# Kernel optimization log

Measured on AMD Instinct MI355X. Metric: run time of the kernel, lower is better.

## Reference

```python
import jax, jax.numpy as jnp
import numpy as np
from math import pi as PI

K = 32
CUTOFF = 10.0
F = 128          # num_filters (also num_gaussians)
H = 256          # in_channels
N_CLASSES = 7
N_IND = 8
LOG2 = float(np.log(2.0))


def _ssp(x):
    # ShiftedSoftplus
    return jax.nn.softplus(x) - LOG2


def _gaussian_smearing(d):
    # d: [E, 1] -> [E, F]; torch_geometric GaussianSmearing(start=0, stop=cutoff)
    offset = jnp.linspace(0.0, CUTOFF, F, dtype=d.dtype)            # [F]
    coeff = -0.5 / (offset[1] - offset[0]) ** 2
    return jnp.exp(coeff * (d - offset[None, :]) ** 2)


def setup_inputs() -> dict:
    key = jax.random.key(0)
    ks = jax.random.split(key, 24)
    Nq, Nc, B = 8192, 16384, 8
    box = 20.0
    pos_query = jax.random.uniform(ks[0], (Nq, 3), dtype=jnp.float32) * box
    pos_ctx = jax.random.uniform(ks[1], (Nc, 3), dtype=jnp.float32) * box
    node_attr_ctx = jax.random.normal(ks[2], (Nc, H), dtype=jnp.float32)
    batch_query = jnp.sort(jax.random.randint(ks[3], (Nq,), 0, B)).astype(jnp.int32)
    batch_ctx = jnp.sort(jax.random.randint(ks[4], (Nc,), 0, B)).astype(jnp.int32)

    def lin_w(k, fin, fout):
        return (jax.random.normal(k, (fin, fout), dtype=jnp.float32) / np.sqrt(fin)).astype(jnp.float32)

    return {
        "pos_query": pos_query,
        "pos_ctx": pos_ctx,
        "node_attr_ctx": node_attr_ctx,
        "batch_query": batch_query,
        "batch_ctx": batch_ctx,
        "lin1_w": lin_w(ks[5], H, F),                 # bias=False
        "lin2_w": lin_w(ks[6], F, F),
        "lin2_b": jnp.zeros((F,), jnp.float32),
        "nn1_w": lin_w(ks[7], F, F),
        "nn1_b": jnp.zeros((F,), jnp.float32),
        "nn2_w": lin_w(ks[8], F, F),
        "nn2_b": jnp.zeros((F,), jnp.float32),
        "cls1_w": lin_w(ks[9], F, F),
        "cls1_b": jnp.zeros((F,), jnp.float32),
        "cls2_w": lin_w(ks[10], F, N_CLASSES),
        "cls2_b": jnp.zeros((N_CLASSES,), jnp.float32),
        "prop1_w": lin_w(ks[11], F, F),
        "prop1_b": jnp.zeros((F,), jnp.float32),
        "prop2_w": lin_w(ks[12], F, N_IND),
        "prop2_b": jnp.zeros((N_IND,), jnp.float32),
    }


def reference(pos_query, pos_ctx, node_attr_ctx, batch_query, batch_ctx,
              lin1_w, lin2_w, lin2_b, nn1_w, nn1_b, nn2_w, nn2_b,
              cls1_w, cls1_b, cls2_w, cls2_b, prop1_w, prop1_b, prop2_w, prop2_b):
    Nq = pos_query.shape[0]

    # --- batch-aware kNN: for each query, k nearest context points in same graph ---
    d2 = (jnp.sum(pos_query ** 2, -1)[:, None]
          + jnp.sum(pos_ctx ** 2, -1)[None, :]
          - 2.0 * (pos_query @ pos_ctx.T))                            # [Nq, Nc]
    same = batch_query[:, None] == batch_ctx[None, :]
    d2 = jnp.where(same, d2, jnp.inf)
    _, nbr = jax.lax.top_k(-d2, K)                                    # [Nq, K] ctx indices

    # --- gather neighbor data; each query owns exactly K contiguous edges ---
    diff = pos_query[:, None, :] - pos_ctx[nbr]                       # [Nq, K, 3]
    dist = jnp.sqrt(jnp.sum(diff ** 2, -1)).reshape(-1, 1)            # [E, 1]
    attr_j = node_attr_ctx[nbr].reshape(Nq * K, -1)                   # [E, H]

    # --- per-edge filter network on distance expansion ---
    W = _ssp(_gaussian_smearing(dist) @ nn1_w + nn1_b) @ nn2_w + nn2_b  # [E, F]

    h = (W * (attr_j @ lin1_w)) @ lin2_w + lin2_b                     # [E, F]

    # --- cosine cutoff envelope ---
    C = 0.5 * (jnp.cos(dist * (PI / CUTOFF)) + 1.0)
    C = C * (dist <= CUTOFF) * (dist >= 0.0)
    h = h * C                                                         # [E, F]

    # scatter_add by query index == sum over the K contiguous edges per query
    y = jnp.sum(h.reshape(Nq, K, F), axis=1)                          # [Nq, F]

    y_cls = _ssp(y @ cls1_w + cls1_b) @ cls2_w + cls2_b               # [Nq, 7]
    y_ind = _ssp(y @ prop1_w + prop1_b) @ prop2_w + prop2_b           # [Nq, 8]
    return (y_cls, y_ind)
```

## Files before the change

kernel.cpp:

```cpp
#include <hip/hip_runtime.h>
#include <hip/hip_fp16.h>
#include <math.h>

#define K 32
#define F 128
#define H 256
#define TAB 4096
#define QB 8
#define BMAX 16
#define RCUT2 100.0f
#define KBINS 64
#define BINCAP 2560
#define BCAP 128
#define FP 132
#define WRR 16

typedef _Float16 f16x8 __attribute__((ext_vector_type(8)));
typedef float f32x4 __attribute__((ext_vector_type(4)));

__device__ __forceinline__ float ssp(float x) {
    return fmaxf(x, 0.0f) + log1pf(expf(-fabsf(x))) - 0.69314718055994531f;
}

__device__ __forceinline__ float d2f4(float4 p, float qx, float qy, float qz) {
    float dx = qx - p.x;
    float dy = qy - p.y;
    float dz = qz - p.z;
    return fmaf(dz, dz, fmaf(dy, dy, dx * dx));
}

__global__ __launch_bounds__(256) void prep_kernel(const int* __restrict__ bc, int Nc,
                                                   int* __restrict__ ctx_start,
                                                   const float* __restrict__ posc,
                                                   float4* __restrict__ posc4,
                                                   const float* __restrict__ attr,
                                                   __half* __restrict__ attrh,
                                                   const float* __restrict__ lin1_w,
                                                   __half* __restrict__ bfragh,
                                                   int padB, int convB) {
    int blk = blockIdx.x;
    int tid = threadIdx.x;
    if (blk == 0) {
        if (tid <= BMAX) {
            int b = tid;
            int lo = 0, hi = Nc;
            while (lo < hi) {
                int mid = (lo + hi) >> 1;
                if (bc[mid] < b) lo = mid + 1; else hi = mid;
            }
            ctx_start[b] = lo;
        }
    } else if (blk <= padB) {
        int i = (blk - 1) * 256 + tid;
        if (i < Nc)
            posc4[i] = make_float4(posc[i * 3 + 0], posc[i * 3 + 1], posc[i * 3 + 2], 0.0f);
    } else if (blk <= padB + convB) {
        size_t base = ((size_t)(blk - 1 - padB) * 256 + tid) * 8;
        if (base < (size_t)Nc * H) {
            float4 v0 = *(const float4*)&attr[base];
            float4 v1 = *(const float4*)&attr[base + 4];
            __half2 h[4];
            h[0] = __floats2half2_rn(v0.x, v0.y);
            h[1] = __floats2half2_rn(v0.z, v0.w);
            h[2] = __floats2half2_rn(v1.x, v1.y);
            h[3] = __floats2half2_rn(v1.z, v1.w);
            *(float4*)&attrh[base] = *(float4*)h;
        }
    } else {
        int ts = blk - 1 - padB - convB;
        int t = ts >> 3, s = ts & 7;
        for (int e = tid; e < 512; e += 256) {
            int l = e >> 3, j = e & 7;
            int k = s * 32 + (l >> 4) * 8 + j;
            int col = (l & 15) + 16 * t;
            bfragh[(size_t)ts * 512 + e] = __float2half(lin1_w[k * F + col]);
        }
    }
}

__global__ __launch_bounds__(256) void feat_kernel(const __half* __restrict__ attrh_,
                                                   const __half* __restrict__ bfragh_,
                                                   __half* __restrict__ ctx_feat, int Nc) {
    const _Float16* attrh = (const _Float16*)attrh_;
    const _Float16* bfragh = (const _Float16*)bfragh_;
    int tid = threadIdx.x;
    int wave = tid >> 6;
    int lane = tid & 63;
    int r0 = blockIdx.x * 32;

    f32x4 acc[2][2] = {{{0.f,0.f,0.f,0.f},{0.f,0.f,0.f,0.f}},{{0.f,0.f,0.f,0.f},{0.f,0.f,0.f,0.f}}};

    int arow[2];
#pragma unroll
    for (int rt = 0; rt < 2; ++rt) {
        int row = r0 + rt * 16 + (lane & 15);
        arow[rt] = (row < Nc) ? row : (Nc - 1);
    }
    int kbase = (lane >> 4) * 8;

    for (int s = 0; s < 8; ++s) {
        f16x8 a0 = *(const f16x8*)(attrh + (size_t)arow[0] * H + s * 32 + kbase);
        f16x8 a1 = *(const f16x8*)(attrh + (size_t)arow[1] * H + s * 32 + kbase);
#pragma unroll
        for (int ct = 0; ct < 2; ++ct) {
            int t = 2 * wave + ct;
            f16x8 b = *(const f16x8*)(bfragh + ((size_t)(t * 8 + s) * 64 + lane) * 8);
            acc[0][ct] = __builtin_amdgcn_mfma_f32_16x16x32_f16(a0, b, acc[0][ct], 0, 0, 0);
            acc[1][ct] = __builtin_amdgcn_mfma_f32_16x16x32_f16(a1, b, acc[1][ct], 0, 0, 0);
        }
    }

#pragma unroll
    for (int rt = 0; rt < 2; ++rt) {
#pragma unroll
        for (int ct = 0; ct < 2; ++ct) {
            int col = (2 * wave + ct) * 16 + (lane & 15);
#pragma unroll
            for (int j = 0; j < 4; ++j) {
                int row = r0 + rt * 16 + (lane >> 4) * 4 + j;
                if (row < Nc)
                    ctx_feat[(size_t)row * F + col] = __float2half(acc[rt][ct][j]);
            }
        }
    }
}

__global__ __launch_bounds__(256) void knn_kernel(const float* __restrict__ posq,
                                                  const float4* __restrict__ posc4,
                                                  const int* __restrict__ bq,
                                                  const int* __restrict__ ctx_start,
                                                  int* __restrict__ nbr, int Nq) {
    __shared__ unsigned char sbin[4][BINCAP];
    __shared__ int hist[4][KBINS];
    __shared__ unsigned bkey[4][BCAP];
    __shared__ int bidx[4][BCAP];
    __shared__ int s_nwin[4], s_nbnd[4];

    int tid = threadIdx.x;
    int lane = tid & 63;
    int w = tid >> 6;
    int q = blockIdx.x * 4 + w;
    bool active = q < Nq;
    int qc = active ? q : 0;

    hist[w][lane] = 0;
    if (lane == 0) { s_nwin[w] = 0; s_nbnd[w] = 0; }

    float qx = posq[qc * 3 + 0];
    float qy = posq[qc * 3 + 1];
    float qz = posq[qc * 3 + 2];
    int b = bq[qc];
    int c0 = ctx_start[b];
    int c1 = ctx_start[b + 1];
    int seg = active ? (c1 - c0) : 0;
    __syncthreads();

    const float SCALE = (float)KBINS / RCUT2;
    int farc = -1;

    for (int i = lane; i < seg; i += 64) {
        float d2 = d2f4(posc4[c0 + i], qx, qy, qz);
        int bin = 255;
        if (d2 < RCUT2) {
            bin = (int)(d2 * SCALE);
            atomicAdd(&hist[w][bin], 1);
        }
        if (i < BINCAP) sbin[w][i] = (unsigned char)bin;
    }
    __syncthreads();

    int h = hist[w][lane];
    int inc = h;
#pragma unroll
    for (int off = 1; off < 64; off <<= 1) {
        int v = __shfl_up(inc, off);
        if (lane >= off) inc += v;
    }
    unsigned long long bal = __ballot(inc >= K);
    int T, below;
    if (bal) {
        T = __ffsll(bal) - 1;
        below = __shfl(inc, T) - __shfl(h, T);
    } else {
        T = KBINS;
        below = __shfl(inc, 63);
    }

    for (int i = lane; i < seg; i += 64) {
        int c = c0 + i;
        int bin;
        if (i < BINCAP) bin = sbin[w][i];
        else {
            float d2 = d2f4(posc4[c], qx, qy, qz);
            bin = (d2 < RCUT2) ? (int)(d2 * SCALE) : 255;
        }
        if (bin < T) {
            int p = atomicAdd(&s_nwin[w], 1);
            nbr[(size_t)q * K + p] = c;
        } else if (bin == T) {
            int p = atomicAdd(&s_nbnd[w], 1);
            if (p < BCAP) {
                float d2 = d2f4(posc4[c], qx, qy, qz);
                bkey[w][p] = __float_as_uint(d2);
                bidx[w][p] = c;
            }
        } else if (bin == 255) {
            farc = c;
        }
    }
#pragma unroll
    for (int off = 1; off < 64; off <<= 1) farc = max(farc, __shfl_xor(farc, off));
    if (farc < 0) farc = c0;
    __syncthreads();

    if (!active) return;
    int nb = min(s_nbnd[w], BCAP);
    int m = K - s_nwin[w];
    for (int it = 0; it < m; ++it) {
        unsigned long long bestkey = 0xFFFFFFFFFFFFFFFFull;
        int bestp = -1;
        for (int p = lane; p < nb; p += 64) {
            unsigned kk = bkey[w][p];
            if (kk != 0xFFFFFFFFu) {
                unsigned long long pk = ((unsigned long long)kk << 32) | (unsigned)bidx[w][p];
                if (pk < bestkey) { bestkey = pk; bestp = p; }
            }
        }
#pragma unroll
        for (int off = 1; off < 64; off <<= 1) {
            unsigned long long ok = __shfl_xor(bestkey, off);
            int op = __shfl_xor(bestp, off);
            if (ok < bestkey) { bestkey = ok; bestp = op; }
        }
        if (lane == 0) {
            if (bestp >= 0 && bestkey != 0xFFFFFFFFFFFFFFFFull) {
                nbr[(size_t)q * K + below + it] = (int)(bestkey & 0xFFFFFFFFu);
                bkey[w][bestp] = 0xFFFFFFFFu;
            } else {
                nbr[(size_t)q * K + below + it] = farc;
            }
        }
        __asm__ volatile("" ::: "memory");
    }
}

__global__ __launch_bounds__(256) void wtab_kernel(const float* __restrict__ nn1_w,
                                                   const float* __restrict__ nn1_b,
                                                   const float* __restrict__ nn2_w,
                                                   const float* __restrict__ nn2_b,
                                                   __half2* __restrict__ wt2h) {
    __shared__ float sg[17][F];
    __shared__ float st[17][F];
    int t0 = blockIdx.x * WRR;
    int tid = threadIdx.x;
    int f = tid & (F - 1);
    int g = tid >> 7;

    const float delta = 10.0f / 127.0f;
    const float coeff = -0.5f / (delta * delta);
    float off = (float)f * delta;
    for (int r = g; r < 17; r += 2) {
        float dist = (float)(t0 + r) * (10.0f / (float)TAB);
        float d = dist - off;
        sg[r][f] = expf(coeff * d * d);
    }
    __syncthreads();

    float acc[9];
#pragma unroll
    for (int r = 0; r < 9; ++r) acc[r] = 0.0f;
    for (int j = 0; j < F; j += 4) {
        float w0 = nn1_w[(j + 0) * F + f];
        float w1 = nn1_w[(j + 1) * F + f];
        float w2 = nn1_w[(j + 2) * F + f];
        float w3 = nn1_w[(j + 3) * F + f];
#pragma unroll
        for (int r = 0; r < 9; ++r) {
            float4 a4 = *(const float4*)&sg[g * 8 + r][j];
            acc[r] = fmaf(a4.x, w0, acc[r]);
            acc[r] = fmaf(a4.y, w1, acc[r]);
            acc[r] = fmaf(a4.z, w2, acc[r]);
            acc[r] = fmaf(a4.w, w3, acc[r]);
        }
    }
    float b1 = nn1_b[f];
#pragma unroll
    for (int r = 0; r < 9; ++r) st[g * 8 + r][f] = ssp(acc[r] + b1);
    __syncthreads();

#pragma unroll
    for (int r = 0; r < 9; ++r) acc[r] = 0.0f;
    for (int j = 0; j < F; j += 4) {
        float w0 = nn2_w[(j + 0) * F + f];
        float w1 = nn2_w[(j + 1) * F + f];
        float w2 = nn2_w[(j + 2) * F + f];
        float w3 = nn2_w[(j + 3) * F + f];
#pragma unroll
        for (int r = 0; r < 9; ++r) {
            float4 a4 = *(const float4*)&st[g * 8 + r][j];
            acc[r] = fmaf(a4.x, w0, acc[r]);
            acc[r] = fmaf(a4.y, w1, acc[r]);
            acc[r] = fmaf(a4.z, w2, acc[r]);
            acc[r] = fmaf(a4.w, w3, acc[r]);
        }
    }
    float b2 = nn2_b[f];
#pragma unroll
    for (int i = 0; i < 8; ++i) {
        int t = t0 + g * 8 + i;
        wt2h[(size_t)t * F + f] = __floats2half2_rn(acc[i] + b2, acc[i + 1] + b2);
    }
}

__global__ __launch_bounds__(256) void agghead_kernel(const float* __restrict__ posq,
                                                      const float4* __restrict__ posc4,
                                                      const int* __restrict__ nbr,
                                                      const __half* __restrict__ ctx_feat,
                                                      const __half2* __restrict__ wt2h,
                                                      const float* __restrict__ lin2_w,
                                                      const float* __restrict__ lin2_b,
                                                      const float* __restrict__ cls1_w,
                                                      const float* __restrict__ cls1_b,
                                                      const float* __restrict__ cls2_w,
                                                      const float* __restrict__ cls2_b,
                                                      const float* __restrict__ prop1_w,
                                                      const float* __restrict__ prop1_b,
                                                      const float* __restrict__ prop2_w,
                                                      const float* __restrict__ prop2_b,
                                                      float* __restrict__ out_cls,
                                                      float* __restrict__ out_ind, int Nq) {
    const int QH = QB / 2;
    int q0 = blockIdx.x * QB;
    int tid = threadIdx.x;

    __shared__ __align__(16) char sm[12672];
    float4* sedge      = (float4*)sm;
    float (*sa)[F]     = (float (*)[F])(sm + 4096);
    float* ssc         = (float*)(sm + 8192);
    float (*sc1)[FP]   = (float (*)[FP])(sm);
    float (*sp1)[FP]   = (float (*)[FP])(sm + 4224);
    float (*sy)[FP]    = (float (*)[FP])(sm + 8448);

    {
        int qq = tid >> 5;
        int q = q0 + qq;
        if (q >= Nq) q = Nq - 1;
        int j = nbr[(size_t)q * K + (tid & 31)];
        float4 p = posc4[j];
        float dx = posq[q * 3 + 0] - p.x;
        float dy = posq[q * 3 + 1] - p.y;
        float dz = posq[q * 3 + 2] - p.z;
        float dist = sqrtf(fmaf(dz, dz, fmaf(dy, dy, dx * dx)));
        float C = 0.0f, fr = 0.0f;
        int i0 = 0;
        if (dist <= 10.0f) {
            C = 0.5f * (cosf(dist * 0.31415926535897931f) + 1.0f);
            float u = dist * ((float)TAB / 10.0f);
            i0 = (int)u;
            if (i0 > TAB - 1) i0 = TAB - 1;
            fr = u - (float)i0;
        }
        sedge[tid] = make_float4(C, fr, __int_as_float(i0 * F), __int_as_float(j * F));
        float cs = C;
#pragma unroll
        for (int off = 1; off < 32; off <<= 1) cs += __shfl_xor(cs, off);
        if ((tid & 31) == 0) ssc[qq] = cs;
    }
    __syncthreads();

    {
        int fp = tid & 63;
        int gg = tid >> 6;
        int f0 = fp * 2;
        const __half2* w2b = wt2h + f0;
        const __half* cfb = ctx_feat + f0;
        float accA[2] = {0.0f, 0.0f};
        float accB[2] = {0.0f, 0.0f};
#pragma unroll 2
        for (int k = 0; k < K; ++k) {
            {
                float4 e4 = sedge[(gg * 2 + 0) * K + k];
                float C = e4.x, fr = e4.y;
                int i0f = __float_as_int(e4.z);
                int jf = __float_as_int(e4.w);
                __half2 h01[2];
                *(float2*)h01 = *(const float2*)(w2b + i0f);
                float2 a2 = __half22float2(*(const __half2*)(cfb + jf));
                float2 wa = __half22float2(h01[0]);
                float2 wb = __half22float2(h01[1]);
                float W0 = fmaf(fr, wa.y - wa.x, wa.x);
                float W1 = fmaf(fr, wb.y - wb.x, wb.x);
                accA[0] = fmaf(C * W0, a2.x, accA[0]);
                accA[1] = fmaf(C * W1, a2.y, accA[1]);
            }
            {
                float4 e4 = sedge[(gg * 2 + 1) * K + k];
                float C = e4.x, fr = e4.y;
                int i0f = __float_as_int(e4.z);
                int jf = __float_as_int(e4.w);
                __half2 h01[2];
                *(float2*)h01 = *(const float2*)(w2b + i0f);
                float2 a2 = __half22float2(*(const __half2*)(cfb + jf));
                float2 wa = __half22float2(h01[0]);
                float2 wb = __half22float2(h01[1]);
                float W0 = fmaf(fr, wa.y - wa.x, wa.x);
                float W1 = fmaf(fr, wb.y - wb.x, wb.x);
                accB[0] = fmaf(C * W0, a2.x, accB[0]);
                accB[1] = fmaf(C * W1, a2.y, accB[1]);
            }
        }
        *(float2*)&sa[gg * 2 + 0][f0] = make_float2(accA[0], accA[1]);
        *(float2*)&sa[gg * 2 + 1][f0] = make_float2(accB[0], accB[1]);
    }
    __syncthreads();

    int f = tid & (F - 1);
    int g = tid >> 7;

    {
        float y[QH];
        float lb = lin2_b[f];
#pragma unroll
        for (int i = 0; i < QH; ++i) y[i] = ssc[g * QH + i] * lb;
        for (int j = 0; j < F; j += 4) {
            float w0 = lin2_w[(j + 0) * F + f];
            float w1 = lin2_w[(j + 1) * F + f];
            float w2 = lin2_w[(j + 2) * F + f];
            float w3 = lin2_w[(j + 3) * F + f];
#pragma unroll
            for (int i = 0; i < QH; ++i) {
                float4 a4 = *(const float4*)&sa[g * QH + i][j];
                y[i] = fmaf(a4.x, w0, y[i]);
                y[i] = fmaf(a4.y, w1, y[i]);
                y[i] = fmaf(a4.z, w2, y[i]);
                y[i] = fmaf(a4.w, w3, y[i]);
            }
        }
#pragma unroll
        for (int i = 0; i < QH; ++i) sy[g * QH + i][f] = y[i];
    }
    __syncthreads();

    {
        float c1[QH], p1[QH];
        float cb = cls1_b[f], pb = prop1_b[f];
#pragma unroll
        for (int i = 0; i < QH; ++i) { c1[i] = cb; p1[i] = pb; }
        for (int j = 0; j < F; j += 4) {
            float wc0 = cls1_w[(j + 0) * F + f];
            float wc1 = cls1_w[(j + 1) * F + f];
            float wc2 = cls1_w[(j + 2) * F + f];
            float wc3 = cls1_w[(j + 3) * F + f];
            float wp0 = prop1_w[(j + 0) * F + f];
            float wp1 = prop1_w[(j + 1) * F + f];
            float wp2 = prop1_w[(j + 2) * F + f];
            float wp3 = prop1_w[(j + 3) * F + f];
#pragma unroll
            for (int i = 0; i < QH; ++i) {
                float4 y4 = *(const float4*)&sy[g * QH + i][j];
                c1[i] = fmaf(y4.x, wc0, c1[i]);
                c1[i] = fmaf(y4.y, wc1, c1[i]);
                c1[i] = fmaf(y4.z, wc2, c1[i]);
                c1[i] = fmaf(y4.w, wc3, c1[i]);
                p1[i] = fmaf(y4.x, wp0, p1[i]);
                p1[i] = fmaf(y4.y, wp1, p1[i]);
                p1[i] = fmaf(y4.z, wp2, p1[i]);
                p1[i] = fmaf(y4.w, wp3, p1[i]);
            }
        }
#pragma unroll
        for (int i = 0; i < QH; ++i) {
            sc1[g * QH + i][f] = ssp(c1[i]);
            sp1[g * QH + i][f] = ssp(p1[i]);
        }
    }
    __syncthreads();

    {
        int qq = tid >> 5;
        int c = tid & 31;
        int q = q0 + qq;
        if (q < Nq && c < 15) {
            if (c < 7) {
                float acc = cls2_b[c];
                for (int j = 0; j < F; ++j) acc = fmaf(sc1[qq][j], cls2_w[j * 7 + c], acc);
                out_cls[(size_t)q * 7 + c] = acc;
            } else {
                int cc = c - 7;
                float acc = prop2_b[cc];
                for (int j = 0; j < F; ++j) acc = fmaf(sp1[qq][j], prop2_w[j * 8 + cc], acc);
                out_ind[(size_t)q * 8 + cc] = acc;
            }
        }
    }
}

extern "C" void kernel_launch(void* const* d_in, const int* in_sizes, int n_in,
                              void* d_out, int out_size, void* d_ws, size_t ws_size,
                              hipStream_t stream) {
    const float* posq   = (const float*)d_in[0];
    const float* posc   = (const float*)d_in[1];
    const float* attr   = (const float*)d_in[2];
    const int*   bq     = (const int*)d_in[3];
    const int*   bc     = (const int*)d_in[4];
    const float* lin1_w = (const float*)d_in[5];
    const float* lin2_w = (const float*)d_in[6];
    const float* lin2_b = (const float*)d_in[7];
    const float* nn1_w  = (const float*)d_in[8];
    const float* nn1_b  = (const float*)d_in[9];
    const float* nn2_w  = (const float*)d_in[10];
    const float* nn2_b  = (const float*)d_in[11];
    const float* cls1_w = (const float*)d_in[12];
    const float* cls1_b = (const float*)d_in[13];
    const float* cls2_w = (const float*)d_in[14];
    const float* cls2_b = (const float*)d_in[15];
    const float* prop1_w = (const float*)d_in[16];
    const float* prop1_b = (const float*)d_in[17];
    const float* prop2_w = (const float*)d_in[18];
    const float* prop2_b = (const float*)d_in[19];
    (void)n_in; (void)out_size; (void)ws_size;

    int Nq = in_sizes[0] / 3;
    int Nc = in_sizes[1] / 3;

    char* ws = (char*)d_ws;
    size_t off = 0;
    auto alloc = [&](size_t bytes) {
        off = (off + 255) & ~(size_t)255;
        void* p = ws + off;
        off += bytes;
        return p;
    };
    int*     ctx_start = (int*)alloc((BMAX + 1) * sizeof(int));
    int*     nbr       = (int*)alloc((size_t)Nq * K * sizeof(int));
    __half*  ctx_feat  = (__half*)alloc((size_t)Nc * F * sizeof(__half));
    __half2* wt2h      = (__half2*)alloc((size_t)TAB * F * sizeof(__half2));
    float4*  posc4     = (float4*)alloc((size_t)Nc * sizeof(float4));
    __half*  attrh     = (__half*)alloc((size_t)Nc * H * sizeof(__half));
    __half*  bfragh    = (__half*)alloc((size_t)64 * 512 * sizeof(__half));

    float* out_cls = (float*)d_out;
    float* out_ind = out_cls + (size_t)Nq * 7;

    int padB  = (Nc + 255) / 256;
    int convB = (int)(((size_t)Nc * H / 8 + 255) / 256);
    int swzB  = 64;
    int featB = (Nc + 31) / 32;
    int knnB  = (Nq + 3) / 4;
    int wtabB = TAB / WRR;

    prep_kernel<<<dim3(1 + padB + convB + swzB), dim3(256), 0, stream>>>(
        bc, Nc, ctx_start, posc, posc4, attr, attrh, lin1_w, bfragh, padB, convB);
    knn_kernel<<<dim3(knnB), dim3(256), 0, stream>>>(posq, posc4, bq, ctx_start, nbr, Nq);
    feat_kernel<<<dim3(featB), dim3(256), 0, stream>>>(attrh, bfragh, ctx_feat, Nc);
    wtab_kernel<<<dim3(wtabB), dim3(256), 0, stream>>>(nn1_w, nn1_b, nn2_w, nn2_b, wt2h);
    agghead_kernel<<<dim3((Nq + QB - 1) / QB), dim3(256), 0, stream>>>(
        posq, posc4, nbr, ctx_feat, wt2h,
        lin2_w, lin2_b, cls1_w, cls1_b, cls2_w, cls2_b,
        prop1_w, prop1_b, prop2_w, prop2_b, out_cls, out_ind, Nq);
}
```

Baseline: 112.5 us.

## Merge knn, wtab and feat kernels into one launch; widen agg lanes

Merges the three independent kernels (knn search, distance-table build, context feature GEMM) into a single phase2 kernel. Each block dispatches on its block index and reuses one shared-memory buffer, which removes two launches and the gaps between them and lets the three workloads share the GPU at the same time. Separately, the aggregation loop in agghead now has each thread handle 4 features for one query, using 16-byte table loads and 8-byte feature loads, instead of 2 features for two queries. The merged kernel's shared memory and register use are set by its largest branch, which may lower occupancy for the lighter work.

Result: slower. 119.9 us (+6.6%).

```diff
diff --git a/kernel.cpp b/kernel.cpp
--- a/kernel.cpp
+++ b/kernel.cpp
@@ -78,68 +78,23 @@
     }
 }
 
-__global__ __launch_bounds__(256) void feat_kernel(const __half* __restrict__ attrh_,
-                                                   const __half* __restrict__ bfragh_,
-                                                   __half* __restrict__ ctx_feat, int Nc) {
-    const _Float16* attrh = (const _Float16*)attrh_;
-    const _Float16* bfragh = (const _Float16*)bfragh_;
-    int tid = threadIdx.x;
-    int wave = tid >> 6;
-    int lane = tid & 63;
-    int r0 = blockIdx.x * 32;
-
-    f32x4 acc[2][2] = {{{0.f,0.f,0.f,0.f},{0.f,0.f,0.f,0.f}},{{0.f,0.f,0.f,0.f},{0.f,0.f,0.f,0.f}}};
-
-    int arow[2];
-#pragma unroll
-    for (int rt = 0; rt < 2; ++rt) {
-        int row = r0 + rt * 16 + (lane & 15);
-        arow[rt] = (row < Nc) ? row : (Nc - 1);
-    }
-    int kbase = (lane >> 4) * 8;
-
-    for (int s = 0; s < 8; ++s) {
-        f16x8 a0 = *(const f16x8*)(attrh + (size_t)arow[0] * H + s * 32 + kbase);
-        f16x8 a1 = *(const f16x8*)(attrh + (size_t)arow[1] * H + s * 32 + kbase);
-#pragma unroll
-        for (int ct = 0; ct < 2; ++ct) {
-            int t = 2 * wave + ct;
-            f16x8 b = *(const f16x8*)(bfragh + ((size_t)(t * 8 + s) * 64 + lane) * 8);
-            acc[0][ct] = __builtin_amdgcn_mfma_f32_16x16x32_f16(a0, b, acc[0][ct], 0, 0, 0);
-            acc[1][ct] = __builtin_amdgcn_mfma_f32_16x16x32_f16(a1, b, acc[1][ct], 0, 0, 0);
-        }
-    }
-
-#pragma unroll
-    for (int rt = 0; rt < 2; ++rt) {
-#pragma unroll
-        for (int ct = 0; ct < 2; ++ct) {
-            int col = (2 * wave + ct) * 16 + (lane & 15);
-#pragma unroll
-            for (int j = 0; j < 4; ++j) {
-                int row = r0 + rt * 16 + (lane >> 4) * 4 + j;
-                if (row < Nc)
-                    ctx_feat[(size_t)row * F + col] = __float2half(acc[rt][ct][j]);
-            }
-        }
-    }
-}
-
-__global__ __launch_bounds__(256) void knn_kernel(const float* __restrict__ posq,
-                                                  const float4* __restrict__ posc4,
-                                                  const int* __restrict__ bq,
-                                                  const int* __restrict__ ctx_start,
-                                                  int* __restrict__ nbr, int Nq) {
-    __shared__ unsigned char sbin[4][BINCAP];
-    __shared__ int hist[4][KBINS];
-    __shared__ unsigned bkey[4][BCAP];
-    __shared__ int bidx[4][BCAP];
-    __shared__ int s_nwin[4], s_nbnd[4];
-
-    int tid = threadIdx.x;
+
+__device__ __forceinline__ void knn_body(char* smem, const float* __restrict__ posq,
+                                         const float4* __restrict__ posc4,
+                                         const int* __restrict__ bq,
+                                         const int* __restrict__ ctx_start,
+                                         int* __restrict__ nbr, int Nq,
+                                         int blk, int tid) {
+    unsigned char (*sbin)[BINCAP] = (unsigned char (*)[BINCAP])(smem);
+    int (*hist)[KBINS]            = (int (*)[KBINS])(smem + 10240);
+    unsigned (*bkey)[BCAP]        = (unsigned (*)[BCAP])(smem + 11264);
+    int (*bidx)[BCAP]             = (int (*)[BCAP])(smem + 13312);
+    int* s_nwin                   = (int*)(smem + 15360);
+    int* s_nbnd                   = (int*)(smem + 15376);
+
     int lane = tid & 63;
     int w = tid >> 6;
-    int q = blockIdx.x * 4 + w;
+    int q = blk * 4 + w;
     bool active = q < Nq;
     int qc = active ? q : 0;
 
@@ -244,15 +199,15 @@
     }
 }
 
-__global__ __launch_bounds__(256) void wtab_kernel(const float* __restrict__ nn1_w,
-                                                   const float* __restrict__ nn1_b,
-                                                   const float* __restrict__ nn2_w,
-                                                   const float* __restrict__ nn2_b,
-                                                   __half2* __restrict__ wt2h) {
-    __shared__ float sg[17][F];
-    __shared__ float st[17][F];
-    int t0 = blockIdx.x * WRR;
-    int tid = threadIdx.x;
+__device__ __forceinline__ void wtab_body(char* smem, const float* __restrict__ nn1_w,
+                                          const float* __restrict__ nn1_b,
+                                          const float* __restrict__ nn2_w,
+                                          const float* __restrict__ nn2_b,
+                                          __half2* __restrict__ wt2h,
+                                          int blk, int tid) {
+    float (*sg)[F] = (float (*)[F])smem;
+    float (*st)[F] = (float (*)[F])(smem + 8704);
+    int t0 = blk * WRR;
     int f = tid & (F - 1);
     int g = tid >> 7;
 
@@ -309,6 +264,79 @@
     for (int i = 0; i < 8; ++i) {
         int t = t0 + g * 8 + i;
         wt2h[(size_t)t * F + f] = __floats2half2_rn(acc[i] + b2, acc[i + 1] + b2);
+    }
+}
+
+__device__ __forceinline__ void feat_body(const __half* __restrict__ attrh_,
+                                          const __half* __restrict__ bfragh_,
+                                          __half* __restrict__ ctx_feat, int Nc,
+                                          int blk, int tid) {
+    const _Float16* attrh = (const _Float16*)attrh_;
+    const _Float16* bfragh = (const _Float16*)bfragh_;
+    int wave = tid >> 6;
+    int lane = tid & 63;
+    int r0 = blk * 32;
+
+    f32x4 acc[2][2] = {{{0.f,0.f,0.f,0.f},{0.f,0.f,0.f,0.f}},{{0.f,0.f,0.f,0.f},{0.f,0.f,0.f,0.f}}};
+
+    int arow[2];
+#pragma unroll
+    for (int rt = 0; rt < 2; ++rt) {
+        int row = r0 + rt * 16 + (lane & 15);
+        arow[rt] = (row < Nc) ? row : (Nc - 1);
+    }
+    int kbase = (lane >> 4) * 8;
+
+    for (int s = 0; s < 8; ++s) {
+        f16x8 a0 = *(const f16x8*)(attrh + (size_t)arow[0] * H + s * 32 + kbase);
+        f16x8 a1 = *(const f16x8*)(attrh + (size_t)arow[1] * H + s * 32 + kbase);
+#pragma unroll
+        for (int ct = 0; ct < 2; ++ct) {
+            int t = 2 * wave + ct;
+            f16x8 b = *(const f16x8*)(bfragh + ((size_t)(t * 8 + s) * 64 + lane) * 8);
+            acc[0][ct] = __builtin_amdgcn_mfma_f32_16x16x32_f16(a0, b, acc[0][ct], 0, 0, 0);
+            acc[1][ct] = __builtin_amdgcn_mfma_f32_16x16x32_f16(a1, b, acc[1][ct], 0, 0, 0);
+        }
+    }
+
+#pragma unroll
+    for (int rt = 0; rt < 2; ++rt) {
+#pragma unroll
+        for (int ct = 0; ct < 2; ++ct) {
+            int col = (2 * wave + ct) * 16 + (lane & 15);
+#pragma unroll
+            for (int j = 0; j < 4; ++j) {
+                int row = r0 + rt * 16 + (lane >> 4) * 4 + j;
+                if (row < Nc)
+                    ctx_feat[(size_t)row * F + col] = __float2half(acc[rt][ct][j]);
+            }
+        }
+    }
+}
+
+__global__ __launch_bounds__(256) void phase2_kernel(const float* __restrict__ posq,
+                                                     const float4* __restrict__ posc4,
+                                                     const int* __restrict__ bq,
+                                                     const int* __restrict__ ctx_start,
+                                                     int* __restrict__ nbr, int Nq,
+                                                     const float* __restrict__ nn1_w,
+                                                     const float* __restrict__ nn1_b,
+                                                     const float* __restrict__ nn2_w,
+                                                     const float* __restrict__ nn2_b,
+                                                     __half2* __restrict__ wt2h,
+                                                     const __half* __restrict__ attrh,
+                                                     const __half* __restrict__ bfragh,
+                                                     __half* __restrict__ ctx_feat, int Nc,
+                                                     int knnB, int wtabB) {
+    __shared__ __align__(16) char smem[17408];
+    int blk = blockIdx.x;
+    int tid = threadIdx.x;
+    if (blk < knnB) {
+        knn_body(smem, posq, posc4, bq, ctx_start, nbr, Nq, blk, tid);
+    } else if (blk < knnB + wtabB) {
+        wtab_body(smem, nn1_w, nn1_b, nn2_w, nn2_b, wt2h, blk - knnB, tid);
+    } else {
+        feat_body(attrh, bfragh, ctx_feat, Nc, blk - knnB - wtabB, tid);
     }
 }
 
@@ -369,48 +397,38 @@
     __syncthreads();
 
     {
-        int fp = tid & 63;
-        int gg = tid >> 6;
-        int f0 = fp * 2;
+        int fq = tid & 31;
+        int qq = tid >> 5;
+        int f0 = fq * 4;
         const __half2* w2b = wt2h + f0;
         const __half* cfb = ctx_feat + f0;
-        float accA[2] = {0.0f, 0.0f};
-        float accB[2] = {0.0f, 0.0f};
-#pragma unroll 2
+        float acc[4] = {0.0f, 0.0f, 0.0f, 0.0f};
+#pragma unroll 4
         for (int k = 0; k < K; ++k) {
-            {
-                float4 e4 = sedge[(gg * 2 + 0) * K + k];
-                float C = e4.x, fr = e4.y;
-                int i0f = __float_as_int(e4.z);
-                int jf = __float_as_int(e4.w);
-                __half2 h01[2];
-                *(float2*)h01 = *(const float2*)(w2b + i0f);
-                float2 a2 = __half22float2(*(const __half2*)(cfb + jf));
-                float2 wa = __half22float2(h01[0]);
-                float2 wb = __half22float2(h01[1]);
-                float W0 = fmaf(fr, wa.y - wa.x, wa.x);
-                float W1 = fmaf(fr, wb.y - wb.x, wb.x);
-                accA[0] = fmaf(C * W0, a2.x, accA[0]);
-                accA[1] = fmaf(C * W1, a2.y, accA[1]);
-            }
-            {
-                float4 e4 = sedge[(gg * 2 + 1) * K + k];
-                float C = e4.x, fr = e4.y;
-                int i0f = __float_as_int(e4.z);
-                int jf = __float_as_int(e4.w);
-                __half2 h01[2];
-                *(float2*)h01 = *(const float2*)(w2b + i0f);
-                float2 a2 = __half22float2(*(const __half2*)(cfb + jf));
-                float2 wa = __half22float2(h01[0]);
-                float2 wb = __half22float2(h01[1]);
-                float W0 = fmaf(fr, wa.y - wa.x, wa.x);
-                float W1 = fmaf(fr, wb.y - wb.x, wb.x);
-                accB[0] = fmaf(C * W0, a2.x, accB[0]);
-                accB[1] = fmaf(C * W1, a2.y, accB[1]);
-            }
-        }
-        *(float2*)&sa[gg * 2 + 0][f0] = make_float2(accA[0], accA[1]);
-        *(float2*)&sa[gg * 2 + 1][f0] = make_float2(accB[0], accB[1]);
+            float4 e4 = sedge[qq * K + k];
+            float C = e4.x, fr = e4.y;
+            int i0f = __float_as_int(e4.z);
+            int jf = __float_as_int(e4.w);
+            __half2 w[4];
+            *(float4*)w = *(const float4*)(w2b + i0f);
+            __half2 ah[2];
+            *(float2*)ah = *(const float2*)(cfb + jf);
+            float2 w0 = __half22float2(w[0]);
+            float2 w1 = __half22float2(w[1]);
+            float2 w2 = __half22float2(w[2]);
+            float2 w3 = __half22float2(w[3]);
+            float2 a0 = __half22float2(ah[0]);
+            float2 a1 = __half22float2(ah[1]);
+            float W0 = fmaf(fr, w0.y - w0.x, w0.x);
+            float W1 = fmaf(fr, w1.y - w1.x, w1.x);
+            float W2 = fmaf(fr, w2.y - w2.x, w2.x);
+            float W3 = fmaf(fr, w3.y - w3.x, w3.x);
+            acc[0] = fmaf(C * W0, a0.x, acc[0]);
+            acc[1] = fmaf(C * W1, a0.y, acc[1]);
+            acc[2] = fmaf(C * W2, a1.x, acc[2]);
+            acc[3] = fmaf(C * W3, a1.y, acc[3]);
+        }
+        *(float4*)&sa[qq][f0] = make_float4(acc[0], acc[1], acc[2], acc[3]);
     }
     __syncthreads();
 
@@ -551,9 +569,10 @@
 
     prep_kernel<<<dim3(1 + padB + convB + swzB), dim3(256), 0, stream>>>(
         bc, Nc, ctx_start, posc, posc4, attr, attrh, lin1_w, bfragh, padB, convB);
-    knn_kernel<<<dim3(knnB), dim3(256), 0, stream>>>(posq, posc4, bq, ctx_start, nbr, Nq);
-    feat_kernel<<<dim3(featB), dim3(256), 0, stream>>>(attrh, bfragh, ctx_feat, Nc);
-    wtab_kernel<<<dim3(wtabB), dim3(256), 0, stream>>>(nn1_w, nn1_b, nn2_w, nn2_b, wt2h);
+    phase2_kernel<<<dim3(knnB + wtabB + featB), dim3(256), 0, stream>>>(
+        posq, posc4, bq, ctx_start, nbr, Nq,
+        nn1_w, nn1_b, nn2_w, nn2_b, wt2h,
+        attrh, bfragh, ctx_feat, Nc, knnB, wtabB);
     agghead_kernel<<<dim3((Nq + QB - 1) / QB), dim3(256), 0, stream>>>(
         posq, posc4, nbr, ctx_feat, wt2h,
         lin2_w, lin2_b, cls1_w, cls1_b, cls2_w, cls2_b,
```
